# Kernel tuning notes

Hardware: AMD Instinct MI355X
Metric: run time of the kernel (lower is better)

## Reference

```python
import jax, jax.numpy as jnp
import numpy as np

B, N, D, H = 2, 2048, 1024, 16
DH = D // H
MASK_VALUE = -1e7


def setup_inputs() -> dict:
    key = jax.random.key(0)
    ks = jax.random.split(key, 8)
    scale = 0.02
    return {
        "queries": jax.random.normal(ks[0], (B, N, D), dtype=jnp.float32),
        "keys": jax.random.normal(ks[1], (B, N, D), dtype=jnp.float32),
        "values": jax.random.normal(ks[2], (B, N, D), dtype=jnp.float32),
        "valid_len": jax.random.randint(ks[3], (B * H,), 1, N + 1, dtype=jnp.int32),
        "Wq": jax.random.normal(ks[4], (D, D), dtype=jnp.float32) * scale,
        "Wk": jax.random.normal(ks[5], (D, D), dtype=jnp.float32) * scale,
        "Wv": jax.random.normal(ks[6], (D, D), dtype=jnp.float32) * scale,
        "Wo": jax.random.normal(ks[7], (D, D), dtype=jnp.float32) * scale,
    }


def reference(queries, keys, values, valid_len, Wq, Wk, Wv, Wo):
    b, n, d = queries.shape
    h, dh = H, d // H

    def split_heads(x):  # (b, n, d) -> (b, h, n, dh)
        return x.reshape(b, n, h, dh).transpose(0, 2, 1, 3)

    q = split_heads(queries @ Wq)
    k = split_heads(keys @ Wk)
    v = split_heads(values @ Wv)

    # (b, h, nq, nk) full score tensor, as in the original naive bmm path
    scores = jnp.einsum("bhqd,bhkd->bhqk", q, k) / jnp.sqrt(jnp.float32(dh))

    # valid_len is 1-D of length b*h; repeat_interleave over queries means the
    # mask depends only on the key index: keep k < valid_len[bh]
    vl = valid_len.reshape(b, h, 1, 1)
    keep = jnp.arange(n)[None, None, None, :] < vl  # (b, h, 1, nk)
    scores = jnp.where(keep, scores, MASK_VALUE)

    attn = jax.nn.softmax(scores, axis=-1)
    heads = jnp.einsum("bhqk,bhkd->bhqd", attn, v)  # (b, h, n, dh)
    out = heads.transpose(0, 2, 1, 3).reshape(b, n, d) @ Wo
    return out
```

## Files before the change

kernel.cpp:

```cpp
#include <hip/hip_runtime.h>

#define B_ 2
#define N_ 2048
#define D_ 1024
#define H_ 16
#define DH_ 64
#define NITEMS 1024

typedef _Float16 half8 __attribute__((ext_vector_type(8)));
typedef _Float16 half4 __attribute__((ext_vector_type(4)));
typedef float f32x4 __attribute__((ext_vector_type(4)));

__device__ __forceinline__ void gl2lds16(const _Float16* g, _Float16* l) {
  __builtin_amdgcn_global_load_lds(
      (const __attribute__((address_space(1))) void*)g,
      (__attribute__((address_space(3))) void*)l, 16, 0, 0);
}

__global__ __launch_bounds__(256) void convert_x_kernel(
    const float* __restrict__ q, const float* __restrict__ k,
    const float* __restrict__ v, _Float16* __restrict__ dst) {
  const float* s = (blockIdx.y == 0) ? q : (blockIdx.y == 1) ? k : v;
  _Float16* d = dst + (size_t)blockIdx.y * ((size_t)B_ * N_ * D_);
  size_t idx = ((size_t)blockIdx.x * 256 + threadIdx.x) * 8;
  float4 a = *(const float4*)(s + idx);
  float4 b = *(const float4*)(s + idx + 4);
  half8 h;
  h[0] = (_Float16)a.x; h[1] = (_Float16)a.y; h[2] = (_Float16)a.z; h[3] = (_Float16)a.w;
  h[4] = (_Float16)b.x; h[5] = (_Float16)b.y; h[6] = (_Float16)b.z; h[7] = (_Float16)b.w;
  *(half8*)(d + idx) = h;
}

__global__ __launch_bounds__(256) void convert_w_kernel(
    const float* __restrict__ Wq, const float* __restrict__ Wk,
    const float* __restrict__ Wv, const float* __restrict__ Wo,
    _Float16* __restrict__ WtAll) {
  const float* W = (blockIdx.z == 0) ? Wq : (blockIdx.z == 1) ? Wk
                  : (blockIdx.z == 2) ? Wv : Wo;
  _Float16* Wt = WtAll + (size_t)blockIdx.z * D_ * D_;
  __shared__ float tile[64][65];
  int k0 = blockIdx.y * 64, n0 = blockIdx.x * 64;
  int tr = threadIdx.x >> 4, tc = threadIdx.x & 15;
#pragma unroll
  for (int i = 0; i < 4; ++i) {
    int r = tr + i * 16;
    float4 va = *(const float4*)(W + (size_t)(k0 + r) * D_ + n0 + tc * 4);
    tile[r][tc * 4 + 0] = va.x; tile[r][tc * 4 + 1] = va.y;
    tile[r][tc * 4 + 2] = va.z; tile[r][tc * 4 + 3] = va.w;
  }
  __syncthreads();
#pragma unroll
  for (int i = 0; i < 4; ++i) {
    int r = tr + i * 16;
    half4 hv;
    hv[0] = (_Float16)tile[tc * 4 + 0][r];
    hv[1] = (_Float16)tile[tc * 4 + 1][r];
    hv[2] = (_Float16)tile[tc * 4 + 2][r];
    hv[3] = (_Float16)tile[tc * 4 + 3][r];
    *(half4*)(Wt + (size_t)(n0 + r) * D_ + k0 + tc * 4) = hv;
  }
}

template <int NT, int MODE>
__global__ __launch_bounds__(256) void gemm_f16_kernel(
    const _Float16* __restrict__ Aall, const _Float16* __restrict__ Btall,
    _Float16* __restrict__ ChAll, float* __restrict__ Cf32) {
  constexpr int BN = NT * 32;
  constexpr int K = D_;
  __shared__ __attribute__((aligned(16))) _Float16 As[128 * 64];
  __shared__ __attribute__((aligned(16))) _Float16 Bs[BN * 64];
  const int z = blockIdx.z;
  const _Float16* A  = Aall  + (size_t)z * ((size_t)B_ * N_ * D_);
  const _Float16* Bt = Btall + (size_t)z * ((size_t)D_ * D_);
  _Float16* Chead = ChAll + (size_t)z * ((size_t)B_ * N_ * D_);

  const int tid = threadIdx.x;
  const int m0 = blockIdx.y * 128, n0 = blockIdx.x * BN;
  const int lane = tid & 63, w = tid >> 6;
  const int quad = lane >> 4, l15 = lane & 15;
  const int wm = (w >> 1) * 64, wn = (w & 1) * (BN / 2);
  const int l7 = l15 & 7;
  f32x4 acc[4][NT] = {};

  for (int kt = 0; kt < K; kt += 64) {
    if (kt) __syncthreads();
#pragma unroll
    for (int p = 0; p < 4; ++p) {
      int c = p * 256 + tid;
      int row = c >> 3, pg = c & 7, gl = pg ^ (row & 7);
      gl2lds16(A + (size_t)(m0 + row) * K + kt + gl * 8, &As[c * 8]);
    }
#pragma unroll
    for (int p = 0; p < NT; ++p) {
      int c = p * 256 + tid;
      int row = c >> 3, pg = c & 7, gl = pg ^ (row & 7);
      gl2lds16(Bt + (size_t)(n0 + row) * K + kt + gl * 8, &Bs[c * 8]);
    }
    __syncthreads();
    half8 af[4][2], bf[NT][2];
#pragma unroll
    for (int mt = 0; mt < 4; ++mt) {
      int row = wm + mt * 16 + l15;
#pragma unroll
      for (int hh = 0; hh < 2; ++hh)
        af[mt][hh] = *(const half8*)&As[row * 64 + (((quad + 4 * hh) ^ l7) * 8)];
    }
#pragma unroll
    for (int nt = 0; nt < NT; ++nt) {
      int row = wn + nt * 16 + l15;
#pragma unroll
      for (int hh = 0; hh < 2; ++hh)
        bf[nt][hh] = *(const half8*)&Bs[row * 64 + (((quad + 4 * hh) ^ l7) * 8)];
    }
#pragma unroll
    for (int hh = 0; hh < 2; ++hh)
#pragma unroll
      for (int mt = 0; mt < 4; ++mt)
#pragma unroll
        for (int nt = 0; nt < NT; ++nt)
          acc[mt][nt] = __builtin_amdgcn_mfma_f32_16x16x32_f16(
              af[mt][hh], bf[nt][hh], acc[mt][nt], 0, 0, 0);
  }

#pragma unroll
  for (int mt = 0; mt < 4; ++mt) {
    int mrow = m0 + wm + mt * 16 + quad * 4;
#pragma unroll
    for (int nt = 0; nt < NT; ++nt) {
      int jcol = n0 + wn + nt * 16 + l15;
#pragma unroll
      for (int r = 0; r < 4; ++r) {
        float val = acc[mt][nt][r];
        int m = mrow + r;
        if (MODE == 0) {
          int b = m >> 11, n = m & (N_ - 1);
          int h = jcol >> 6, dh = jcol & (DH_ - 1);
          Chead[((((size_t)(b * H_ + h)) * N_ + n) * DH_) + dh] = (_Float16)val;
        } else {
          Cf32[(size_t)m * D_ + jcol] = val;
        }
      }
    }
  }
}

__global__ __launch_bounds__(256) void transpose_v_kernel(
    const _Float16* __restrict__ Vh, _Float16* __restrict__ VtG) {
  __shared__ float Ls[64][65];
  int bh = blockIdx.y, k0 = blockIdx.x * 64;
  int tid = threadIdx.x;
  const _Float16* src = Vh + (size_t)bh * N_ * DH_;
#pragma unroll
  for (int p = 0; p < 2; ++p) {
    int c = p * 256 + tid, row = c >> 3, pg = c & 7;
    half8 hv = *(const half8*)(src + (size_t)(k0 + row) * DH_ + pg * 8);
#pragma unroll
    for (int u = 0; u < 8; ++u) Ls[row][pg * 8 + u] = (float)hv[u];
  }
  __syncthreads();
  _Float16* dst = VtG + (size_t)bh * N_ * DH_;
#pragma unroll
  for (int p = 0; p < 2; ++p) {
    int c = p * 256 + tid, dh = c >> 3, pg = c & 7;
    half8 hv;
#pragma unroll
    for (int u = 0; u < 8; ++u) hv[u] = (_Float16)Ls[pg * 8 + u][dh];
    *(half8*)(dst + (size_t)dh * N_ + k0 + pg * 8) = hv;
  }
}

__global__ void sort_heads_kernel(const int* __restrict__ vlen,
                                  int* __restrict__ order, int* __restrict__ ctr) {
  int i = threadIdx.x;
  if (i == 0) *ctr = 0;
  if (i < B_ * H_) {
    int vi = vlen[i], rank = 0;
    for (int j = 0; j < B_ * H_; ++j) {
      int vj = vlen[j];
      if (vj > vi || (vj == vi && j < i)) ++rank;
    }
    order[rank] = i;
  }
}

__global__ __launch_bounds__(256, 4) void attn_kernel(
    const _Float16* __restrict__ Qh, const _Float16* __restrict__ Kh,
    const _Float16* __restrict__ VtG, const int* __restrict__ vlen,
    _Float16* __restrict__ Hd, const int* __restrict__ order,
    int* __restrict__ ctr) {
  __shared__ __attribute__((aligned(16))) _Float16 Ks[2][64 * 64];
  __shared__ __attribute__((aligned(16))) _Float16 Vt[2][64 * 64];
  __shared__ int sh_item;
  const int tid = threadIdx.x, lane = tid & 63, w = tid >> 6;
  const int quad = lane >> 4, l15 = lane & 15;
  const int sw  = (quad ^ (l15 & 7)) * 8;
  const int sw2 = ((quad + 4) ^ (l15 & 7)) * 8;
  const float sc2 = 0.125f * 1.44269504088896f;
  const half4 ones = {(_Float16)1, (_Float16)1, (_Float16)1, (_Float16)1};

  while (true) {
    if (tid == 0) sh_item = atomicAdd(ctr, 1);
    __syncthreads();
    const int item = sh_item;
    if (item >= NITEMS) return;
    const int bh = order[item >> 5];
    const int q0 = (item & 31) * 64;
    const int b = bh >> 4, h = bh & (H_ - 1);
    const int vl = vlen[bh];
    const int KT = (vl + 63) >> 6;
    const _Float16* Qb = Qh  + (size_t)bh * N_ * DH_;
    const _Float16* Kb = Kh  + (size_t)bh * N_ * DH_;
    const _Float16* Vb = VtG + (size_t)bh * N_ * DH_;

    const half8 qb0 = *(const half8*)(Qb + (size_t)(q0 + w * 16 + l15) * DH_ + quad * 8);
    const half8 qb1 = *(const half8*)(Qb + (size_t)(q0 + w * 16 + l15) * DH_ + 32 + quad * 8);

    half8 kpre[2], vpre[2];
    auto prefetch = [&](int k0k) {
#pragma unroll
      for (int p = 0; p < 2; ++p) {
        int c = p * 256 + tid;
        int row = c >> 3, pg = c & 7;
        kpre[p] = *(const half8*)(Kb + (size_t)(k0k + row) * DH_ + (pg ^ (row & 7)) * 8);
        vpre[p] = *(const half8*)(Vb + (size_t)row * N_ + k0k + pg * 8);
      }
    };
    auto commit = [&](int buf) {
#pragma unroll
      for (int p = 0; p < 2; ++p) {
        int c = p * 256 + tid;
        int row = c >> 3, pg = c & 7;
        *(half8*)&Ks[buf][c * 8] = kpre[p];
        int j0 = (pg * 2) ^ (row & 15), j1 = (pg * 2 + 1) ^ (row & 15);
        half4 lo = {vpre[p][0], vpre[p][1], vpre[p][2], vpre[p][3]};
        half4 hi = {vpre[p][4], vpre[p][5], vpre[p][6], vpre[p][7]};
        *(half4*)&Vt[buf][row * 64 + j0 * 4] = lo;
        *(half4*)&Vt[buf][row * 64 + j1 * 4] = hi;
      }
    };

    prefetch(0);
    commit(0);
    if (KT > 1) prefetch(64);
    __syncthreads();

    f32x4 Oacc[4] = {};
    f32x4 lacc = {};

    for (int kt = 0; kt < KT; ++kt) {
      const int cur = kt & 1;
      if (kt + 1 < KT) commit(1 - cur);
      if (kt + 2 < KT) prefetch((kt + 2) * 64);

      f32x4 s[4];
#pragma unroll
      for (int nt = 0; nt < 4; ++nt) {
        int r = nt * 16 + l15;
        half8 ka0 = *(const half8*)&Ks[cur][r * 64 + sw];
        half8 ka1 = *(const half8*)&Ks[cur][r * 64 + sw2];
        f32x4 c = {};
        c = __builtin_amdgcn_mfma_f32_16x16x32_f16(ka0, qb0, c, 0, 0, 0);
        c = __builtin_amdgcn_mfma_f32_16x16x32_f16(ka1, qb1, c, 0, 0, 0);
        s[nt] = c;
      }
      const int k0k = kt * 64;
      half4 pf[4];
      if (k0k + 64 <= vl) {
#pragma unroll
        for (int nt = 0; nt < 4; ++nt)
#pragma unroll
          for (int r = 0; r < 4; ++r)
            pf[nt][r] = (_Float16)exp2f(s[nt][r] * sc2);
      } else {
#pragma unroll
        for (int nt = 0; nt < 4; ++nt) {
          int keyb = k0k + nt * 16 + quad * 4;
#pragma unroll
          for (int r = 0; r < 4; ++r) {
            float p = exp2f(s[nt][r] * sc2);
            pf[nt][r] = (keyb + r < vl) ? (_Float16)p : (_Float16)0.f;
          }
        }
      }
#pragma unroll
      for (int nt = 0; nt < 4; ++nt) {
        lacc = __builtin_amdgcn_mfma_f32_16x16x16f16(ones, pf[nt], lacc, 0, 0, 0);
#pragma unroll
        for (int dt = 0; dt < 4; ++dt) {
          int dh = dt * 16 + l15;
          half4 va = *(const half4*)&Vt[cur][dh * 64 + (((nt * 4 + quad) ^ l15) << 2)];
          Oacc[dt] = __builtin_amdgcn_mfma_f32_16x16x16f16(va, pf[nt], Oacc[dt], 0, 0, 0);
        }
      }
      __syncthreads();
    }

    float inv_l = 1.0f / lacc[0];
    int q = q0 + w * 16 + l15;
    _Float16* out = Hd + ((size_t)(b * N_ + q)) * D_ + h * DH_;
#pragma unroll
    for (int dt = 0; dt < 4; ++dt) {
      half4 o;
#pragma unroll
      for (int r = 0; r < 4; ++r) o[r] = (_Float16)(Oacc[dt][r] * inv_l);
      *(half4*)(out + dt * 16 + quad * 4) = o;
    }
  }
}

extern "C" void kernel_launch(void* const* d_in, const int* in_sizes, int n_in,
                              void* d_out, int out_size, void* d_ws, size_t ws_size,
                              hipStream_t stream) {
  const float* q  = (const float*)d_in[0];
  const float* k  = (const float*)d_in[1];
  const float* v  = (const float*)d_in[2];
  const int*   vl = (const int*)d_in[3];
  const float* Wq = (const float*)d_in[4];
  const float* Wk = (const float*)d_in[5];
  const float* Wv = (const float*)d_in[6];
  const float* Wo = (const float*)d_in[7];

  const size_t XSZ = (size_t)B_ * N_ * D_;
  const size_t WSZ = (size_t)D_ * D_;
  _Float16* ws = (_Float16*)d_ws;
  _Float16* Xf = ws;
  _Float16* Wt = Xf + 3 * XSZ;
  _Float16* Qh = Wt + 4 * WSZ;
  _Float16* Hd = Qh + 3 * XSZ;
  int* ctr   = (int*)(Hd + XSZ);
  int* order = ctr + 1;
  _Float16* VtG = Xf;

  convert_x_kernel<<<dim3(2048, 3), 256, 0, stream>>>(q, k, v, Xf);
  convert_w_kernel<<<dim3(16, 16, 4), 256, 0, stream>>>(Wq, Wk, Wv, Wo, Wt);

  gemm_f16_kernel<4, 0><<<dim3(D_ / 128, 32, 3), 256, 0, stream>>>(
      Xf, Wt, Qh, nullptr);

  transpose_v_kernel<<<dim3(N_ / 64, B_ * H_), 256, 0, stream>>>(
      Qh + 2 * XSZ, VtG);
  sort_heads_kernel<<<1, 64, 0, stream>>>(vl, order, ctr);

  attn_kernel<<<dim3(512), 256, 0, stream>>>(
      Qh, Qh + XSZ, VtG, vl, Hd, order, ctr);

  gemm_f16_kernel<2, 1><<<dim3(D_ / 64, 32, 1), 256, 0, stream>>>(
      Hd, Wt + 3 * WSZ, nullptr, (float*)d_out);
}
```

Before: 241.5 us.

## Double-buffer GEMM K-tiles and replace atomic attention scheduling with static pairing

The GEMM kernel now stages 32-wide K slices into two LDS buffers, prefetching the next slice while MFMAs run on the current one. This replaces the single 64-wide buffer that synchronised twice per iteration, at the cost of more loop iterations and a new swizzle. The attention kernel drops its atomic work counter and gives each of the 512 blocks a fixed pair of items: item blockIdx and item NITEMS-1-blockIdx. Over heads sorted by length, this pairs long work with short work, removing the atomic and the counter reset but giving up dynamic load balancing.

Result: no change. 240.8 us (-0.3%).

```diff
diff --git a/kernel.cpp b/kernel.cpp
--- a/kernel.cpp
+++ b/kernel.cpp
@@ -67,8 +67,8 @@
     _Float16* __restrict__ ChAll, float* __restrict__ Cf32) {
   constexpr int BN = NT * 32;
   constexpr int K = D_;
-  __shared__ __attribute__((aligned(16))) _Float16 As[128 * 64];
-  __shared__ __attribute__((aligned(16))) _Float16 Bs[BN * 64];
+  __shared__ __attribute__((aligned(16))) _Float16 As[2][128 * 32];
+  __shared__ __attribute__((aligned(16))) _Float16 Bs[2][BN * 32];
   const int z = blockIdx.z;
   const _Float16* A  = Aall  + (size_t)z * ((size_t)B_ * N_ * D_);
   const _Float16* Bt = Btall + (size_t)z * ((size_t)D_ * D_);
@@ -79,47 +79,50 @@
   const int lane = tid & 63, w = tid >> 6;
   const int quad = lane >> 4, l15 = lane & 15;
   const int wm = (w >> 1) * 64, wn = (w & 1) * (BN / 2);
-  const int l7 = l15 & 7;
+  const int sr = tid >> 2, sc4 = tid & 3;
   f32x4 acc[4][NT] = {};
 
-  for (int kt = 0; kt < K; kt += 64) {
-    if (kt) __syncthreads();
-#pragma unroll
-    for (int p = 0; p < 4; ++p) {
-      int c = p * 256 + tid;
-      int row = c >> 3, pg = c & 7, gl = pg ^ (row & 7);
-      gl2lds16(A + (size_t)(m0 + row) * K + kt + gl * 8, &As[c * 8]);
-    }
-#pragma unroll
-    for (int p = 0; p < NT; ++p) {
-      int c = p * 256 + tid;
-      int row = c >> 3, pg = c & 7, gl = pg ^ (row & 7);
-      gl2lds16(Bt + (size_t)(n0 + row) * K + kt + gl * 8, &Bs[c * 8]);
-    }
-    __syncthreads();
-    half8 af[4][2], bf[NT][2];
+  auto stage = [&](int kt, int buf) {
+#pragma unroll
+    for (int p = 0; p < 2; ++p) {
+      int row = sr + p * 64;
+      int gl = sc4 ^ ((row >> 1) & 3);
+      gl2lds16(A + (size_t)(m0 + row) * K + kt + gl * 8,
+               &As[buf][(row * 4 + sc4) * 8]);
+    }
+#pragma unroll
+    for (int p = 0; p < NT / 2; ++p) {
+      int row = sr + p * 64;
+      int gl = sc4 ^ ((row >> 1) & 3);
+      gl2lds16(Bt + (size_t)(n0 + row) * K + kt + gl * 8,
+               &Bs[buf][(row * 4 + sc4) * 8]);
+    }
+  };
+
+  stage(0, 0);
+  __syncthreads();
+
+  for (int kt = 0; kt < K / 32; ++kt) {
+    const int cur = kt & 1;
+    if (kt + 1 < K / 32) stage((kt + 1) * 32, 1 - cur);
+    half8 af[4], bf[NT];
 #pragma unroll
     for (int mt = 0; mt < 4; ++mt) {
       int row = wm + mt * 16 + l15;
-#pragma unroll
-      for (int hh = 0; hh < 2; ++hh)
-        af[mt][hh] = *(const half8*)&As[row * 64 + (((quad + 4 * hh) ^ l7) * 8)];
+      af[mt] = *(const half8*)&As[cur][(row * 4 + (quad ^ ((row >> 1) & 3))) * 8];
     }
 #pragma unroll
     for (int nt = 0; nt < NT; ++nt) {
       int row = wn + nt * 16 + l15;
-#pragma unroll
-      for (int hh = 0; hh < 2; ++hh)
-        bf[nt][hh] = *(const half8*)&Bs[row * 64 + (((quad + 4 * hh) ^ l7) * 8)];
-    }
-#pragma unroll
-    for (int hh = 0; hh < 2; ++hh)
-#pragma unroll
-      for (int mt = 0; mt < 4; ++mt)
-#pragma unroll
-        for (int nt = 0; nt < NT; ++nt)
-          acc[mt][nt] = __builtin_amdgcn_mfma_f32_16x16x32_f16(
-              af[mt][hh], bf[nt][hh], acc[mt][nt], 0, 0, 0);
+      bf[nt] = *(const half8*)&Bs[cur][(row * 4 + (quad ^ ((row >> 1) & 3))) * 8];
+    }
+#pragma unroll
+    for (int mt = 0; mt < 4; ++mt)
+#pragma unroll
+      for (int nt = 0; nt < NT; ++nt)
+        acc[mt][nt] = __builtin_amdgcn_mfma_f32_16x16x32_f16(
+            af[mt], bf[nt], acc[mt][nt], 0, 0, 0);
+    __syncthreads();
   }
 
 #pragma unroll
@@ -170,9 +173,8 @@
 }
 
 __global__ void sort_heads_kernel(const int* __restrict__ vlen,
-                                  int* __restrict__ order, int* __restrict__ ctr) {
+                                  int* __restrict__ order) {
   int i = threadIdx.x;
-  if (i == 0) *ctr = 0;
   if (i < B_ * H_) {
     int vi = vlen[i], rank = 0;
     for (int j = 0; j < B_ * H_; ++j) {
@@ -186,11 +188,9 @@
 __global__ __launch_bounds__(256, 4) void attn_kernel(
     const _Float16* __restrict__ Qh, const _Float16* __restrict__ Kh,
     const _Float16* __restrict__ VtG, const int* __restrict__ vlen,
-    _Float16* __restrict__ Hd, const int* __restrict__ order,
-    int* __restrict__ ctr) {
+    _Float16* __restrict__ Hd, const int* __restrict__ order) {
   __shared__ __attribute__((aligned(16))) _Float16 Ks[2][64 * 64];
   __shared__ __attribute__((aligned(16))) _Float16 Vt[2][64 * 64];
-  __shared__ int sh_item;
   const int tid = threadIdx.x, lane = tid & 63, w = tid >> 6;
   const int quad = lane >> 4, l15 = lane & 15;
   const int sw  = (quad ^ (l15 & 7)) * 8;
@@ -198,11 +198,9 @@
   const float sc2 = 0.125f * 1.44269504088896f;
   const half4 ones = {(_Float16)1, (_Float16)1, (_Float16)1, (_Float16)1};
 
-  while (true) {
-    if (tid == 0) sh_item = atomicAdd(ctr, 1);
-    __syncthreads();
-    const int item = sh_item;
-    if (item >= NITEMS) return;
+#pragma unroll 1
+  for (int half_ = 0; half_ < 2; ++half_) {
+    const int item = half_ ? (NITEMS - 1 - (int)blockIdx.x) : (int)blockIdx.x;
     const int bh = order[item >> 5];
     const int q0 = (item & 31) * 64;
     const int b = bh >> 4, h = bh & (H_ - 1);
@@ -239,6 +237,7 @@
       }
     };
 
+    if (half_) __syncthreads();
     prefetch(0);
     commit(0);
     if (KT > 1) prefetch(64);
@@ -327,8 +326,7 @@
   _Float16* Wt = Xf + 3 * XSZ;
   _Float16* Qh = Wt + 4 * WSZ;
   _Float16* Hd = Qh + 3 * XSZ;
-  int* ctr   = (int*)(Hd + XSZ);
-  int* order = ctr + 1;
+  int* order = (int*)(Hd + XSZ);
   _Float16* VtG = Xf;
 
   convert_x_kernel<<<dim3(2048, 3), 256, 0, stream>>>(q, k, v, Xf);
@@ -339,10 +337,10 @@
 
   transpose_v_kernel<<<dim3(N_ / 64, B_ * H_), 256, 0, stream>>>(
       Qh + 2 * XSZ, VtG);
-  sort_heads_kernel<<<1, 64, 0, stream>>>(vl, order, ctr);
+  sort_heads_kernel<<<1, 64, 0, stream>>>(vl, order);
 
   attn_kernel<<<dim3(512), 256, 0, stream>>>(
-      Qh, Qh + XSZ, VtG, vl, Hd, order, ctr);
+      Qh, Qh + XSZ, VtG, vl, Hd, order);
 
   gemm_f16_kernel<2, 1><<<dim3(D_ / 64, 32, 1), 256, 0, stream>>>(
       Hd, Wt + 3 * WSZ, nullptr, (float*)d_out);
```
